# Performance work log

Measured on AMD Instinct MI355X. Metric: run time of the kernel, lower is better.

The kernel has to match this reference:

```python
import jax, jax.numpy as jnp
import numpy as np

EPS = 1e-5
NHEAD = 8
TOP_K = 2


def _layernorm(x, g, b):
    m = jnp.mean(x, axis=-1, keepdims=True)
    v = jnp.mean((x - m) ** 2, axis=-1, keepdims=True)
    return (x - m) * jax.lax.rsqrt(v + EPS) * g + b


def setup_inputs() -> dict:
    S, D, F, E = 4096, 512, 2048, 8
    key = jax.random.key(0)
    ks = jax.random.split(key, 18)
    std = 0.02
    return {
        "src": jax.random.normal(ks[0], (S, D), jnp.float32),
        "in_proj_w": std * jax.random.normal(ks[1], (3 * D, D), jnp.float32),
        "in_proj_b": jnp.zeros((3 * D,), jnp.float32),
        "out_proj_w": std * jax.random.normal(ks[2], (D, D), jnp.float32),
        "out_proj_b": jnp.zeros((D,), jnp.float32),
        "ln1_g": jnp.ones((D,), jnp.float32),
        "ln1_b": jnp.zeros((D,), jnp.float32),
        "ln2_g": jnp.ones((D,), jnp.float32),
        "ln2_b": jnp.zeros((D,), jnp.float32),
        "gate_w": std * jax.random.normal(ks[3], (E, D), jnp.float32),
        "gate_b": jnp.zeros((E,), jnp.float32),
        "w1": std * jax.random.normal(ks[4], (E, F, D), jnp.float32),
        "b1": jnp.zeros((E, F), jnp.float32),
        "w2": std * jax.random.normal(ks[5], (E, F, D), jnp.float32),
        "b2": jnp.zeros((E, F), jnp.float32),
        "wo": std * jax.random.normal(ks[6], (E, D, F), jnp.float32),
        "bo": jnp.zeros((E, D), jnp.float32),
    }


def _sa_block(x, in_proj_w, in_proj_b, out_proj_w, out_proj_b):
    # x: [S, D] unbatched sequence (torch MultiheadAttention unbatched path)
    S, D = x.shape
    hd = D // NHEAD
    qkv = x @ in_proj_w.T + in_proj_b              # [S, 3D]
    q, k, v = jnp.split(qkv, 3, axis=-1)
    q = q.reshape(S, NHEAD, hd)
    k = k.reshape(S, NHEAD, hd)
    v = v.reshape(S, NHEAD, hd)
    scores = jnp.einsum("shd,thd->hst", q, k) / jnp.sqrt(jnp.float32(hd))
    attn = jax.nn.softmax(scores, axis=-1)         # [H, S, S]
    out = jnp.einsum("hst,thd->shd", attn, v).reshape(S, D)
    return out @ out_proj_w.T + out_proj_b


def _ff_block(x, gate_w, gate_b, w1, b1, w2, b2, wo, bo):
    # top-k gated SwiGLU MoE; gate probs are softmax, NOT renormalized after topk
    T = x.shape[0]
    E = w1.shape[0]
    gates = jax.nn.softmax(x @ gate_w.T + gate_b, axis=-1)      # [T, E]
    top_scores, top_idx = jax.lax.top_k(gates, TOP_K)            # [T, k]
    combine = jnp.zeros((T, E), x.dtype).at[
        jnp.arange(T)[:, None], top_idx].add(top_scores)         # [T, E]
    out = jnp.zeros_like(x)
    for e in range(E):  # small fixed expert count
        h = jax.nn.silu(x @ w1[e].T + b1[e]) * (x @ w2[e].T + b2[e])
        out = out + combine[:, e:e + 1] * (h @ wo[e].T + bo[e])
    return out


def reference(src, in_proj_w, in_proj_b, out_proj_w, out_proj_b,
              ln1_g, ln1_b, ln2_g, ln2_b,
              gate_w, gate_b, w1, b1, w2, b2, wo, bo):
    # norm_first pre-norm residual layer, dropout=0 (eval)
    x = src
    x = x + _sa_block(_layernorm(x, ln1_g, ln1_b),
                      in_proj_w, in_proj_b, out_proj_w, out_proj_b)
    x = x + _ff_block(_layernorm(x, ln2_g, ln2_b),
                      gate_w, gate_b, w1, b1, w2, b2, wo, bo)
    return x
```

## Files before the change

### kernel.cpp

```cpp
#include <hip/hip_runtime.h>
#include <hip/hip_bf16.h>
#include <math.h>

#define SQ   4096
#define DM   512
#define NH   8
#define HDIM 64
#define FF   2048
#define NE   8

typedef unsigned short u16;
typedef unsigned int   u32;
typedef __attribute__((ext_vector_type(8))) __bf16 bf16x8;
typedef __attribute__((ext_vector_type(4))) float  f32x4;

__device__ __forceinline__ float bf2f(u16 v) {
    union { u32 i; float f; } c; c.i = ((u32)v) << 16; return c.f;
}
__device__ __forceinline__ u16 f2bf(float f) {
    union { float f; u32 i; } c; c.f = f; u32 u = c.i;
    return (u16)((u + 0x7fffu + ((u >> 16) & 1u)) >> 16);
}

#define BM 128
#define BN 128
#define BK 32
#define BKP 40

__global__ __launch_bounds__(256) void gemm_split(
    const u16* __restrict__ Ahi, const u16* __restrict__ Alo, int lda,
    const u16* __restrict__ Bhi, const u16* __restrict__ Blo, int ldb,
    int M, int N, int K,
    const float* __restrict__ bias,
    const float* __restrict__ resid, int ldres,
    u16* __restrict__ Chi, u16* __restrict__ Clo,
    float* __restrict__ Cf, int ldc, int mode)
{
    __shared__ __align__(16) u16 Ash[BM * BKP], Asl[BM * BKP];
    __shared__ __align__(16) u16 Bsh[BN * BKP], Bsl[BN * BKP];
    const int tid  = threadIdx.x;
    const int wave = tid >> 6;
    const int lane = tid & 63;
    const int quad = lane >> 4;
    const int l16  = lane & 15;
    const int bm = blockIdx.x * BM;
    const int bn = blockIdx.y * BN;
    const int wm = (wave & 1) * 64;
    const int wn = (wave >> 1) * 64;

    f32x4 acc[4][4];
#pragma unroll
    for (int i = 0; i < 4; i++)
#pragma unroll
        for (int j = 0; j < 4; j++)
#pragma unroll
            for (int r = 0; r < 4; r++) acc[i][j][r] = 0.0f;

    for (int k0 = 0; k0 < K; k0 += BK) {
#pragma unroll
        for (int i = 0; i < 2; i++) {
            int c = tid + i * 256;
            int row = c >> 2;
            int col = (c & 3) << 3;
            int ga = bm + row, gb2 = bn + row;
            uint4 vah = make_uint4(0u,0u,0u,0u), val = vah, vbh = vah, vbl = vah;
            if (ga < M) {
                vah = *(const uint4*)(Ahi + (size_t)ga * lda + k0 + col);
                val = *(const uint4*)(Alo + (size_t)ga * lda + k0 + col);
            }
            if (gb2 < N) {
                vbh = *(const uint4*)(Bhi + (size_t)gb2 * ldb + k0 + col);
                vbl = *(const uint4*)(Blo + (size_t)gb2 * ldb + k0 + col);
            }
            *(uint4*)(Ash + row * BKP + col) = vah;
            *(uint4*)(Asl + row * BKP + col) = val;
            *(uint4*)(Bsh + row * BKP + col) = vbh;
            *(uint4*)(Bsl + row * BKP + col) = vbl;
        }
        __syncthreads();
        bf16x8 ah[4], al[4], bh[4], bl[4];
#pragma unroll
        for (int i = 0; i < 4; i++) {
            ah[i] = *(const bf16x8*)(Ash + (wm + i * 16 + l16) * BKP + quad * 8);
            al[i] = *(const bf16x8*)(Asl + (wm + i * 16 + l16) * BKP + quad * 8);
        }
#pragma unroll
        for (int j = 0; j < 4; j++) {
            bh[j] = *(const bf16x8*)(Bsh + (wn + j * 16 + l16) * BKP + quad * 8);
            bl[j] = *(const bf16x8*)(Bsl + (wn + j * 16 + l16) * BKP + quad * 8);
        }
#pragma unroll
        for (int i = 0; i < 4; i++)
#pragma unroll
            for (int j = 0; j < 4; j++) {
                acc[i][j] = __builtin_amdgcn_mfma_f32_16x16x32_bf16(ah[i], bh[j], acc[i][j], 0,0,0);
                acc[i][j] = __builtin_amdgcn_mfma_f32_16x16x32_bf16(ah[i], bl[j], acc[i][j], 0,0,0);
                acc[i][j] = __builtin_amdgcn_mfma_f32_16x16x32_bf16(al[i], bh[j], acc[i][j], 0,0,0);
            }
        __syncthreads();
    }

#pragma unroll
    for (int i = 0; i < 4; i++)
#pragma unroll
        for (int j = 0; j < 4; j++)
#pragma unroll
            for (int r = 0; r < 4; r++) {
                int row = bm + wm + i * 16 + quad * 4 + r;
                int col = bn + wn + j * 16 + l16;
                if (row >= M || col >= N) continue;
                float v = acc[i][j][r] + (bias ? bias[col] : 0.0f);
                size_t idx = (size_t)row * ldc + col;
                if (mode == 0) {
                    u16 hb = f2bf(v);
                    Chi[idx] = hb;
                    Clo[idx] = f2bf(v - bf2f(hb));
                } else {
                    if (resid) v += resid[(size_t)row * ldres + col];
                    Cf[idx] = v;
                }
            }
}

__global__ __launch_bounds__(256) void moe12_all(
    const u16* __restrict__ A, int lda,
    const int* __restrict__ idxl, const int* __restrict__ cnt,
    const int* __restrict__ off,
    const float* __restrict__ w1, const float* __restrict__ b1,
    const float* __restrict__ w2, const float* __restrict__ b2,
    u16* __restrict__ H)
{
    const int bmg = blockIdx.x * BM;
    if (bmg >= off[NE]) return;
    int e = 0;
    while (e < NE - 1 && bmg >= off[e + 1]) e++;
    const int M   = cnt[e];
    const int bml = bmg - off[e];
    if (bml >= M) return;
    const float* B1 = w1 + (size_t)e * FF * DM;
    const float* B2 = w2 + (size_t)e * FF * DM;
    const int*   rl = idxl + e * SQ;

    __shared__ __align__(16) u16 As[BM * BKP], Bs1[BN * BKP], Bs2[BN * BKP];
    const int tid  = threadIdx.x;
    const int wave = tid >> 6;
    const int lane = tid & 63;
    const int quad = lane >> 4;
    const int l16  = lane & 15;
    const int bn = blockIdx.y * BN;
    const int wm = (wave & 1) * 64;
    const int wn = (wave >> 1) * 64;

    f32x4 acc1[4][4], acc2[4][4];
#pragma unroll
    for (int i = 0; i < 4; i++)
#pragma unroll
        for (int j = 0; j < 4; j++)
#pragma unroll
            for (int r = 0; r < 4; r++) { acc1[i][j][r] = 0.0f; acc2[i][j][r] = 0.0f; }

    for (int k0 = 0; k0 < DM; k0 += BK) {
#pragma unroll
        for (int i = 0; i < 2; i++) {
            int c = tid + i * 256;
            int row = c >> 2;
            int col = (c & 3) << 3;
            uint4 va = make_uint4(0u,0u,0u,0u);
            int lr = bml + row;
            if (lr < M) {
                int ar = rl[lr];
                va = *(const uint4*)(A + (size_t)ar * lda + k0 + col);
            }
            *(uint4*)(As + row * BKP + col) = va;
        }
#pragma unroll
        for (int i = 0; i < 4; i++) {
            int c = tid + i * 256;
            int row = c >> 3;
            int col = (c & 7) << 2;
            float4 v1 = *(const float4*)(B1 + (size_t)(bn + row) * DM + k0 + col);
            float4 v2 = *(const float4*)(B2 + (size_t)(bn + row) * DM + k0 + col);
            ushort4 h1, h2;
            h1.x = f2bf(v1.x); h1.y = f2bf(v1.y); h1.z = f2bf(v1.z); h1.w = f2bf(v1.w);
            h2.x = f2bf(v2.x); h2.y = f2bf(v2.y); h2.z = f2bf(v2.z); h2.w = f2bf(v2.w);
            *(ushort4*)(Bs1 + row * BKP + col) = h1;
            *(ushort4*)(Bs2 + row * BKP + col) = h2;
        }
        __syncthreads();
        bf16x8 af[4], b1f[4], b2f[4];
#pragma unroll
        for (int i = 0; i < 4; i++)
            af[i] = *(const bf16x8*)(As + (wm + i * 16 + l16) * BKP + quad * 8);
#pragma unroll
        for (int j = 0; j < 4; j++) {
            b1f[j] = *(const bf16x8*)(Bs1 + (wn + j * 16 + l16) * BKP + quad * 8);
            b2f[j] = *(const bf16x8*)(Bs2 + (wn + j * 16 + l16) * BKP + quad * 8);
        }
#pragma unroll
        for (int i = 0; i < 4; i++)
#pragma unroll
            for (int j = 0; j < 4; j++) {
                acc1[i][j] = __builtin_amdgcn_mfma_f32_16x16x32_bf16(af[i], b1f[j], acc1[i][j], 0,0,0);
                acc2[i][j] = __builtin_amdgcn_mfma_f32_16x16x32_bf16(af[i], b2f[j], acc2[i][j], 0,0,0);
            }
        __syncthreads();
    }

#pragma unroll
    for (int i = 0; i < 4; i++)
#pragma unroll
        for (int j = 0; j < 4; j++)
#pragma unroll
            for (int r = 0; r < 4; r++) {
                int rowl = bml + wm + i * 16 + quad * 4 + r;
                if (rowl >= M) continue;
                int col = bn + wn + j * 16 + l16;
                float g1 = acc1[i][j][r] + b1[e * FF + col];
                float g2 = acc2[i][j][r] + b2[e * FF + col];
                float s  = g1 / (1.0f + __expf(-g1));
                H[(size_t)(off[e] + rowl) * FF + col] = f2bf(s * g2);
            }
}

__global__ __launch_bounds__(256) void moe_y_all(
    const u16* __restrict__ H,
    const float* __restrict__ wo, const float* __restrict__ bo,
    const int* __restrict__ idxl, const float* __restrict__ cw,
    const int* __restrict__ cnt, const int* __restrict__ off,
    float* __restrict__ out)
{
    const int bmg = blockIdx.x * BM;
    if (bmg >= off[NE]) return;
    int e = 0;
    while (e < NE - 1 && bmg >= off[e + 1]) e++;
    const int M   = cnt[e];
    const int bml = bmg - off[e];
    if (bml >= M) return;
    const float* B = wo + (size_t)e * DM * FF;

    __shared__ __align__(16) u16 As[BM * BKP], Bs[BN * BKP];
    const int tid  = threadIdx.x;
    const int wave = tid >> 6;
    const int lane = tid & 63;
    const int quad = lane >> 4;
    const int l16  = lane & 15;
    const int bn = blockIdx.y * BN;
    const int wm = (wave & 1) * 64;
    const int wn = (wave >> 1) * 64;

    f32x4 acc[4][4];
#pragma unroll
    for (int i = 0; i < 4; i++)
#pragma unroll
        for (int j = 0; j < 4; j++)
#pragma unroll
            for (int r = 0; r < 4; r++) acc[i][j][r] = 0.0f;

    for (int k0 = 0; k0 < FF; k0 += BK) {
#pragma unroll
        for (int i = 0; i < 2; i++) {
            int c = tid + i * 256;
            int row = c >> 2;
            int col = (c & 3) << 3;
            uint4 va = *(const uint4*)(H + (size_t)(bmg + row) * FF + k0 + col);
            *(uint4*)(As + row * BKP + col) = va;
        }
#pragma unroll
        for (int i = 0; i < 4; i++) {
            int c = tid + i * 256;
            int row = c >> 3;
            int col = (c & 7) << 2;
            float4 v = *(const float4*)(B + (size_t)(bn + row) * FF + k0 + col);
            ushort4 h;
            h.x = f2bf(v.x); h.y = f2bf(v.y); h.z = f2bf(v.z); h.w = f2bf(v.w);
            *(ushort4*)(Bs + row * BKP + col) = h;
        }
        __syncthreads();
        bf16x8 af[4], bf[4];
#pragma unroll
        for (int i = 0; i < 4; i++)
            af[i] = *(const bf16x8*)(As + (wm + i * 16 + l16) * BKP + quad * 8);
#pragma unroll
        for (int j = 0; j < 4; j++)
            bf[j] = *(const bf16x8*)(Bs + (wn + j * 16 + l16) * BKP + quad * 8);
#pragma unroll
        for (int i = 0; i < 4; i++)
#pragma unroll
            for (int j = 0; j < 4; j++)
                acc[i][j] = __builtin_amdgcn_mfma_f32_16x16x32_bf16(af[i], bf[j], acc[i][j], 0,0,0);
        __syncthreads();
    }

#pragma unroll
    for (int i = 0; i < 4; i++)
#pragma unroll
        for (int j = 0; j < 4; j++)
#pragma unroll
            for (int r = 0; r < 4; r++) {
                int rowl = bml + wm + i * 16 + quad * 4 + r;
                if (rowl >= M) continue;
                int col = bn + wn + j * 16 + l16;
                int tok = idxl[e * SQ + rowl];
                float wgt = cw[e * SQ + rowl];
                atomicAdd(out + (size_t)tok * DM + col,
                          wgt * (acc[i][j][r] + bo[e * DM + col]));
            }
}

#define KP 72
#define SCL 0.18033688011112042f
__global__ __launch_bounds__(256) void flash_attn(
    const u16* __restrict__ qh, const u16* __restrict__ ql,
    const u16* __restrict__ vth, const u16* __restrict__ vtl,
    u16* __restrict__ oh, u16* __restrict__ ol)
{
    __shared__ __align__(16) u16 Ksh[64*KP], Ksl[64*KP], Vsh[64*KP], Vsl[64*KP];
    const int tid  = threadIdx.x;
    const int wave = tid >> 6;
    const int lane = tid & 63;
    const int quad = lane >> 4;
    const int l16  = lane & 15;
    const int h    = blockIdx.y;
    const int qbase = blockIdx.x * 64 + wave * 16;

    u16* const Pwh = Ksh + wave * (16 * KP);
    u16* const Pwl = Ksl + wave * (16 * KP);

    bf16x8 aqh[2], aql[2];
#pragma unroll
    for (int kk = 0; kk < 2; kk++) {
        size_t off = (size_t)(qbase + l16) * (3*DM) + h*HDIM + kk*32 + quad*8;
        aqh[kk] = *(const bf16x8*)(qh + off);
        aql[kk] = *(const bf16x8*)(ql + off);
    }

    float m_[4], l_[4];
    f32x4 o_[4];
#pragma unroll
    for (int r = 0; r < 4; r++) { m_[r] = -1e30f; l_[r] = 0.0f; }
#pragma unroll
    for (int nd = 0; nd < 4; nd++)
#pragma unroll
        for (int r = 0; r < 4; r++) o_[nd][r] = 0.0f;

    for (int jt = 0; jt < SQ / 64; jt++) {
#pragma unroll
        for (int i = 0; i < 2; i++) {
            int c = tid + i * 256;
            int r = c >> 3;
            int co = (c & 7) << 3;
            size_t koff = (size_t)(jt*64 + r) * (3*DM) + DM + h*HDIM + co;
            size_t voff = (size_t)(h*HDIM + r) * SQ + jt*64 + co;
            *(uint4*)(Ksh + r*KP + co) = *(const uint4*)(qh + koff);
            *(uint4*)(Ksl + r*KP + co) = *(const uint4*)(ql + koff);
            *(uint4*)(Vsh + r*KP + co) = *(const uint4*)(vth + voff);
            *(uint4*)(Vsl + r*KP + co) = *(const uint4*)(vtl + voff);
        }
        __syncthreads();

        f32x4 s[4];
#pragma unroll
        for (int jn = 0; jn < 4; jn++) {
            f32x4 z;
#pragma unroll
            for (int r = 0; r < 4; r++) z[r] = 0.0f;
#pragma unroll
            for (int kk = 0; kk < 2; kk++) {
                bf16x8 kh = *(const bf16x8*)(Ksh + (jn*16 + l16)*KP + kk*32 + quad*8);
                bf16x8 kl = *(const bf16x8*)(Ksl + (jn*16 + l16)*KP + kk*32 + quad*8);
                z = __builtin_amdgcn_mfma_f32_16x16x32_bf16(aqh[kk], kh, z, 0,0,0);
                z = __builtin_amdgcn_mfma_f32_16x16x32_bf16(aqh[kk], kl, z, 0,0,0);
                z = __builtin_amdgcn_mfma_f32_16x16x32_bf16(aql[kk], kh, z, 0,0,0);
            }
#pragma unroll
            for (int r = 0; r < 4; r++) z[r] *= SCL;
            s[jn] = z;
        }
        __syncthreads();

        float mx[4], al2[4], rs[4];
#pragma unroll
        for (int r = 0; r < 4; r++)
            mx[r] = fmaxf(fmaxf(s[0][r], s[1][r]), fmaxf(s[2][r], s[3][r]));
#pragma unroll
        for (int r = 0; r < 4; r++) {
#pragma unroll
            for (int o2 = 1; o2 < 16; o2 <<= 1)
                mx[r] = fmaxf(mx[r], __shfl_xor(mx[r], o2));
            float nm = fmaxf(m_[r], mx[r]);
            al2[r] = exp2f(m_[r] - nm);
            m_[r] = nm;
            rs[r] = 0.0f;
        }
#pragma unroll
        for (int jn = 0; jn < 4; jn++)
#pragma unroll
            for (int r = 0; r < 4; r++) {
                float p = exp2f(s[jn][r] - m_[r]);
                s[jn][r] = p;
                rs[r] += p;
            }
#pragma unroll
        for (int r = 0; r < 4; r++) {
#pragma unroll
            for (int o2 = 1; o2 < 16; o2 <<= 1)
                rs[r] += __shfl_xor(rs[r], o2);
            l_[r] = l_[r] * al2[r] + rs[r];
        }
#pragma unroll
        for (int nd = 0; nd < 4; nd++)
#pragma unroll
            for (int r = 0; r < 4; r++) o_[nd][r] *= al2[r];
#pragma unroll
        for (int jn = 0; jn < 4; jn++)
#pragma unroll
            for (int r = 0; r < 4; r++) {
                float p = s[jn][r];
                u16 ph = f2bf(p);
                int pidx = (quad*4 + r)*KP + jn*16 + l16;
                Pwh[pidx] = ph;
                Pwl[pidx] = f2bf(p - bf2f(ph));
            }

        bf16x8 ph[2], pl[2];
#pragma unroll
        for (int kk = 0; kk < 2; kk++) {
            ph[kk] = *(const bf16x8*)(Pwh + l16*KP + kk*32 + quad*8);
            pl[kk] = *(const bf16x8*)(Pwl + l16*KP + kk*32 + quad*8);
        }
#pragma unroll
        for (int nd = 0; nd < 4; nd++) {
#pragma unroll
            for (int kk = 0; kk < 2; kk++) {
                bf16x8 vh = *(const bf16x8*)(Vsh + (nd*16 + l16)*KP + kk*32 + quad*8);
                bf16x8 vl = *(const bf16x8*)(Vsl + (nd*16 + l16)*KP + kk*32 + quad*8);
                o_[nd] = __builtin_amdgcn_mfma_f32_16x16x32_bf16(ph[kk], vh, o_[nd], 0,0,0);
                o_[nd] = __builtin_amdgcn_mfma_f32_16x16x32_bf16(ph[kk], vl, o_[nd], 0,0,0);
                o_[nd] = __builtin_amdgcn_mfma_f32_16x16x32_bf16(pl[kk], vh, o_[nd], 0,0,0);
            }
        }
        __syncthreads();
    }

#pragma unroll
    for (int nd = 0; nd < 4; nd++)
#pragma unroll
        for (int r = 0; r < 4; r++) {
            int row = qbase + quad*4 + r;
            int col = h*HDIM + nd*16 + l16;
            float w = o_[nd][r] / l_[r];
            u16 hb = f2bf(w);
            oh[(size_t)row * DM + col] = hb;
            ol[(size_t)row * DM + col] = f2bf(w - bf2f(hb));
        }
}

__global__ __launch_bounds__(256) void ln1_split(
    const float* __restrict__ x, const float* __restrict__ g,
    const float* __restrict__ b, u16* __restrict__ ohi, u16* __restrict__ olo)
{
    const int row = blockIdx.x;
    const int tid = threadIdx.x;
    float v0 = x[(size_t)row * DM + tid];
    float v1 = x[(size_t)row * DM + tid + 256];
    float s = v0 + v1, sq = v0*v0 + v1*v1;
#pragma unroll
    for (int o = 1; o < 64; o <<= 1) { s += __shfl_xor(s, o); sq += __shfl_xor(sq, o); }
    __shared__ float ss[4], ssq[4];
    if ((tid & 63) == 0) { ss[tid>>6] = s; ssq[tid>>6] = sq; }
    __syncthreads();
    s  = ss[0]+ss[1]+ss[2]+ss[3];
    sq = ssq[0]+ssq[1]+ssq[2]+ssq[3];
    float m = s * (1.0f/DM);
    float rstd = rsqrtf(sq*(1.0f/DM) - m*m + 1e-5f);
    float y0 = (v0-m)*rstd*g[tid]     + b[tid];
    float y1 = (v1-m)*rstd*g[tid+256] + b[tid+256];
    u16 h0 = f2bf(y0), h1 = f2bf(y1);
    ohi[(size_t)row*DM + tid]       = h0;  olo[(size_t)row*DM + tid]       = f2bf(y0 - bf2f(h0));
    ohi[(size_t)row*DM + tid + 256] = h1;  olo[(size_t)row*DM + tid + 256] = f2bf(y1 - bf2f(h1));
}

__global__ __launch_bounds__(256) void ln_kernel(
    const float* __restrict__ x, const float* __restrict__ g,
    const float* __restrict__ b, u16* __restrict__ out)
{
    const int row = blockIdx.x;
    const int tid = threadIdx.x;
    float v0 = x[(size_t)row * DM + tid];
    float v1 = x[(size_t)row * DM + tid + 256];
    float s = v0 + v1, sq = v0*v0 + v1*v1;
#pragma unroll
    for (int o = 1; o < 64; o <<= 1) { s += __shfl_xor(s, o); sq += __shfl_xor(sq, o); }
    __shared__ float ss[4], ssq[4];
    if ((tid & 63) == 0) { ss[tid>>6] = s; ssq[tid>>6] = sq; }
    __syncthreads();
    s  = ss[0]+ss[1]+ss[2]+ss[3];
    sq = ssq[0]+ssq[1]+ssq[2]+ssq[3];
    float m = s * (1.0f/DM);
    float rstd = rsqrtf(sq*(1.0f/DM) - m*m + 1e-5f);
    out[(size_t)row*DM + tid]       = f2bf((v0-m)*rstd*g[tid]     + b[tid]);
    out[(size_t)row*DM + tid + 256] = f2bf((v1-m)*rstd*g[tid+256] + b[tid+256]);
}

__global__ __launch_bounds__(256) void transpose_v2(
    const u16* __restrict__ qh, const u16* __restrict__ ql,
    u16* __restrict__ vth, u16* __restrict__ vtl)
{
    __shared__ u16 Th[64 * 66], Tl[64 * 66];
    const int t0  = blockIdx.x * 64;
    const int hd0 = blockIdx.y * 64;
    const int tid = threadIdx.x;
#pragma unroll
    for (int k = 0; k < 16; k++) {
        int idx = tid + k * 256;
        int r = idx >> 6, j = idx & 63;
        size_t src = (size_t)(t0 + r) * (3*DM) + 2*DM + hd0 + j;
        Th[r * 66 + j] = qh[src];
        Tl[r * 66 + j] = ql[src];
    }
    __syncthreads();
#pragma unroll
    for (int k = 0; k < 16; k++) {
        int idx = tid + k * 256;
        int r = idx >> 6, c2 = idx & 63;
        size_t dst = (size_t)(hd0 + r) * SQ + t0 + c2;
        vth[dst] = Th[c2 * 66 + r];
        vtl[dst] = Tl[c2 * 66 + r];
    }
}

__global__ __launch_bounds__(256) void gate_route(
    const float* __restrict__ x1, const float* __restrict__ g,
    const float* __restrict__ b, const float* __restrict__ gw,
    const float* __restrict__ gb,
    int* __restrict__ cnt, int* __restrict__ idxl, float* __restrict__ cw)
{
    const int token = blockIdx.x * 4 + (threadIdx.x >> 6);
    const int lane  = threadIdx.x & 63;
    const float* xr = x1 + (size_t)token * DM;
    float v[8];
#pragma unroll
    for (int i = 0; i < 8; i++) v[i] = xr[lane*8 + i];
    float s = 0.f, sq = 0.f;
#pragma unroll
    for (int i = 0; i < 8; i++) { s += v[i]; sq += v[i]*v[i]; }
#pragma unroll
    for (int o = 1; o < 64; o <<= 1) { s += __shfl_xor(s, o); sq += __shfl_xor(sq, o); }
    float m = s * (1.0f/DM);
    float rstd = rsqrtf(sq*(1.0f/DM) - m*m + 1e-5f);
    float xn[8];
#pragma unroll
    for (int i = 0; i < 8; i++)
        xn[i] = (v[i]-m)*rstd*g[lane*8+i] + b[lane*8+i];
    float logit[8];
#pragma unroll
    for (int e = 0; e < 8; e++) {
        float t = 0.f;
#pragma unroll
        for (int i = 0; i < 8; i++) t += xn[i] * gw[e*DM + lane*8 + i];
#pragma unroll
        for (int o = 1; o < 64; o <<= 1) t += __shfl_xor(t, o);
        logit[e] = t + gb[e];
    }
    if (lane == 0) {
        float mx = -1e30f;
        for (int e = 0; e < 8; e++) mx = fmaxf(mx, logit[e]);
        float den = 0.f, p[8];
        for (int e = 0; e < 8; e++) { p[e] = __expf(logit[e] - mx); den += p[e]; }
        for (int e = 0; e < 8; e++) p[e] /= den;
        int i1 = 0;
        for (int e = 1; e < 8; e++) if (p[e] > p[i1]) i1 = e;
        int i2 = -1;
        for (int e = 0; e < 8; e++) { if (e == i1) continue; if (i2 < 0 || p[e] > p[i2]) i2 = e; }
        int s1 = atomicAdd(&cnt[i1], 1);
        idxl[i1*SQ + s1] = token;  cw[i1*SQ + s1] = p[i1];
        int s2 = atomicAdd(&cnt[i2], 1);
        idxl[i2*SQ + s2] = token;  cw[i2*SQ + s2] = p[i2];
    }
}

__global__ __launch_bounds__(256) void cvt_split_w(
    const float* __restrict__ w, u16* __restrict__ wh, u16* __restrict__ wl, int n)
{
    int i = blockIdx.x * 256 + threadIdx.x;
    if (i < n) {
        float v = w[i];
        u16 h = f2bf(v);
        wh[i] = h;
        wl[i] = f2bf(v - bf2f(h));
    }
}

__global__ __launch_bounds__(64) void zero_cnt(int* cnt)
{
    if (threadIdx.x < NE) cnt[threadIdx.x] = 0;
}

__global__ __launch_bounds__(64) void make_off(const int* __restrict__ cnt,
                                              int* __restrict__ off)
{
    if (threadIdx.x == 0) {
        int a = 0;
        for (int e = 0; e < NE; e++) {
            off[e] = a;
            a += ((cnt[e] + 127) >> 7) << 7;
        }
        off[NE] = a;
    }
}

__global__ __launch_bounds__(256) void init_out(
    const float* __restrict__ x1, float* __restrict__ out)
{
    int i = blockIdx.x * 256 + threadIdx.x;
    ((float4*)out)[i] = ((const float4*)x1)[i];
}

__global__ __launch_bounds__(256) void sentinel_kernel(float* out, float v, int n)
{
    int i = blockIdx.x * 256 + threadIdx.x;
    if (i < n) out[i] = v;
}
__global__ __launch_bounds__(256) void scrub_kernel(float* out, int n)
{
    int i = blockIdx.x * 256 + threadIdx.x;
    if (i < n) { float v = out[i]; if (!isfinite(v)) out[i] = 777.0f; }
}

extern "C" void kernel_launch(void* const* d_in, const int* in_sizes, int n_in,
                              void* d_out, int out_size, void* d_ws, size_t ws_size,
                              hipStream_t stream)
{
    const float* src        = (const float*)d_in[0];
    const float* in_proj_w  = (const float*)d_in[1];
    const float* in_proj_b  = (const float*)d_in[2];
    const float* out_proj_w = (const float*)d_in[3];
    const float* out_proj_b = (const float*)d_in[4];
    const float* ln1_g      = (const float*)d_in[5];
    const float* ln1_b      = (const float*)d_in[6];
    const float* ln2_g      = (const float*)d_in[7];
    const float* ln2_b      = (const float*)d_in[8];
    const float* gate_w     = (const float*)d_in[9];
    const float* gate_b     = (const float*)d_in[10];
    const float* w1         = (const float*)d_in[11];
    const float* b1         = (const float*)d_in[12];
    const float* w2         = (const float*)d_in[13];
    const float* b2         = (const float*)d_in[14];
    const float* wo         = (const float*)d_in[15];
    const float* bo         = (const float*)d_in[16];
    float* out = (float*)d_out;

    const size_t MB = (size_t)1 << 20;
    const size_t ROUTE = 512 * 1024;
    const size_t NEED = ROUTE + 44 * MB;
    if (ws_size < NEED) {
        sentinel_kernel<<<(SQ*DM)/256, 256, 0, stream>>>(out, 333.0f, SQ*DM);
        return;
    }

    char* ws = (char*)d_ws;
    int*   cnt  = (int*)ws;
    int*   offp = (int*)(ws + 64);
    int*   idxl = (int*)(ws + 1024);
    float* cw   = (float*)(ws + 1024 + 128*1024);
    char*  base = ws + ROUTE;
    u16* xln1h = (u16*)(base);
    u16* xln1l = (u16*)(base + 4*MB);
    u16* attnh = (u16*)(base);
    u16* attnl = (u16*)(base + 4*MB);
    u16* qkvh  = (u16*)(base + 8*MB);
    u16* qkvl  = (u16*)(base + 20*MB);
    float* x1  = (float*)(base + 8*MB);
    u16* vth   = (u16*)(base + 32*MB);
    u16* vtl   = (u16*)(base + 36*MB);
    u16* xln2  = (u16*)(base + 36*MB);
    u16* Hbuf  = (u16*)(base);
    u16* wph   = (u16*)(base + 40*MB);
    u16* wpl   = (u16*)(base + 40*MB + 1536*1024);
    u16* woh   = (u16*)(base + 43*MB);
    u16* wol   = (u16*)(base + 43*MB + 512*1024);

    cvt_split_w<<<(3*DM*DM)/256, 256, 0, stream>>>(in_proj_w,  wph, wpl, 3*DM*DM);
    cvt_split_w<<<(DM*DM)/256,   256, 0, stream>>>(out_proj_w, woh, wol, DM*DM);

    ln1_split<<<SQ, 256, 0, stream>>>(src, ln1_g, ln1_b, xln1h, xln1l);
    gemm_split<<<dim3(32, 12), 256, 0, stream>>>(
        xln1h, xln1l, DM, wph, wpl, DM, SQ, 3*DM, DM,
        in_proj_b, nullptr, 0, qkvh, qkvl, nullptr, 3*DM, 0);
    transpose_v2<<<dim3(SQ/64, DM/64), 256, 0, stream>>>(qkvh, qkvl, vth, vtl);
    flash_attn<<<dim3(SQ/64, NH), 256, 0, stream>>>(qkvh, qkvl, vth, vtl, attnh, attnl);
    gemm_split<<<dim3(32, 4), 256, 0, stream>>>(
        attnh, attnl, DM, woh, wol, DM, SQ, DM, DM,
        out_proj_b, src, DM, nullptr, nullptr, x1, DM, 1);

    ln_kernel<<<SQ, 256, 0, stream>>>(x1, ln2_g, ln2_b, xln2);
    zero_cnt<<<1, 64, 0, stream>>>(cnt);
    gate_route<<<SQ/4, 256, 0, stream>>>(x1, ln2_g, ln2_b, gate_w, gate_b,
                                         cnt, idxl, cw);
    make_off<<<1, 64, 0, stream>>>(cnt, offp);
    init_out<<<(SQ*DM/4)/256, 256, 0, stream>>>(x1, out);
    moe12_all<<<dim3(72, 16), 256, 0, stream>>>(
        xln2, DM, idxl, cnt, offp, w1, b1, w2, b2, Hbuf);
    moe_y_all<<<dim3(72, 4), 256, 0, stream>>>(
        Hbuf, wo, bo, idxl, cw, cnt, offp, out);

    scrub_kernel<<<(SQ*DM)/256, 256, 0, stream>>>(out, SQ*DM);
}
```

Before: 835.7 us.

## Split flash attention over KV sequence into two partitions with combine kernel

Adds a split-KV (flash-decoding style) variant of the attention kernel that launches twice as many blocks, each covering half the key range. Each block writes unnormalized partial outputs plus running max and sum to workspace, and a new combine kernel merges the two partitions and performs the hi/lo bf16 split. This targets low occupancy, since 512 blocks underfill the GPU. The cost is an extra fp32 round-trip of partial outputs and one more launch, and the path only runs when the workspace is at least 61MB beyond the routing area.

```diff
diff --git a/kernel.cpp b/kernel.cpp
--- a/kernel.cpp
+++ b/kernel.cpp
@@ -309,10 +309,14 @@
 
 #define KP 72
 #define SCL 0.18033688011112042f
-__global__ __launch_bounds__(256) void flash_attn(
+
+template <int SPLIT>
+__device__ __forceinline__ void flash_body(
     const u16* __restrict__ qh, const u16* __restrict__ ql,
     const u16* __restrict__ vth, const u16* __restrict__ vtl,
-    u16* __restrict__ oh, u16* __restrict__ ol)
+    u16* __restrict__ oh, u16* __restrict__ ol,
+    float* __restrict__ Opart, float* __restrict__ mpart,
+    float* __restrict__ lpart)
 {
     __shared__ __align__(16) u16 Ksh[64*KP], Ksl[64*KP], Vsh[64*KP], Vsl[64*KP];
     const int tid  = threadIdx.x;
@@ -321,6 +325,7 @@
     const int quad = lane >> 4;
     const int l16  = lane & 15;
     const int h    = blockIdx.y;
+    const int z    = (SPLIT > 1) ? blockIdx.z : 0;
     const int qbase = blockIdx.x * 64 + wave * 16;
 
     u16* const Pwh = Ksh + wave * (16 * KP);
@@ -343,7 +348,8 @@
 #pragma unroll
         for (int r = 0; r < 4; r++) o_[nd][r] = 0.0f;
 
-    for (int jt = 0; jt < SQ / 64; jt++) {
+    const int NT = SQ / 64 / SPLIT;
+    for (int jt = z * NT; jt < (z + 1) * NT; jt++) {
 #pragma unroll
         for (int i = 0; i < 2; i++) {
             int c = tid + i * 256;
@@ -361,20 +367,20 @@
         f32x4 s[4];
 #pragma unroll
         for (int jn = 0; jn < 4; jn++) {
-            f32x4 z;
-#pragma unroll
-            for (int r = 0; r < 4; r++) z[r] = 0.0f;
+            f32x4 zz;
+#pragma unroll
+            for (int r = 0; r < 4; r++) zz[r] = 0.0f;
 #pragma unroll
             for (int kk = 0; kk < 2; kk++) {
                 bf16x8 kh = *(const bf16x8*)(Ksh + (jn*16 + l16)*KP + kk*32 + quad*8);
                 bf16x8 kl = *(const bf16x8*)(Ksl + (jn*16 + l16)*KP + kk*32 + quad*8);
-                z = __builtin_amdgcn_mfma_f32_16x16x32_bf16(aqh[kk], kh, z, 0,0,0);
-                z = __builtin_amdgcn_mfma_f32_16x16x32_bf16(aqh[kk], kl, z, 0,0,0);
-                z = __builtin_amdgcn_mfma_f32_16x16x32_bf16(aql[kk], kh, z, 0,0,0);
-            }
-#pragma unroll
-            for (int r = 0; r < 4; r++) z[r] *= SCL;
-            s[jn] = z;
+                zz = __builtin_amdgcn_mfma_f32_16x16x32_bf16(aqh[kk], kh, zz, 0,0,0);
+                zz = __builtin_amdgcn_mfma_f32_16x16x32_bf16(aqh[kk], kl, zz, 0,0,0);
+                zz = __builtin_amdgcn_mfma_f32_16x16x32_bf16(aql[kk], kh, zz, 0,0,0);
+            }
+#pragma unroll
+            for (int r = 0; r < 4; r++) zz[r] *= SCL;
+            s[jn] = zz;
         }
         __syncthreads();
 
@@ -442,17 +448,81 @@
         __syncthreads();
     }
 
-#pragma unroll
-    for (int nd = 0; nd < 4; nd++)
-#pragma unroll
-        for (int r = 0; r < 4; r++) {
-            int row = qbase + quad*4 + r;
-            int col = h*HDIM + nd*16 + l16;
-            float w = o_[nd][r] / l_[r];
-            u16 hb = f2bf(w);
-            oh[(size_t)row * DM + col] = hb;
-            ol[(size_t)row * DM + col] = f2bf(w - bf2f(hb));
-        }
+    if (SPLIT == 1) {
+#pragma unroll
+        for (int nd = 0; nd < 4; nd++)
+#pragma unroll
+            for (int r = 0; r < 4; r++) {
+                int row = qbase + quad*4 + r;
+                int col = h*HDIM + nd*16 + l16;
+                float w = o_[nd][r] / l_[r];
+                u16 hb = f2bf(w);
+                oh[(size_t)row * DM + col] = hb;
+                ol[(size_t)row * DM + col] = f2bf(w - bf2f(hb));
+            }
+    } else {
+#pragma unroll
+        for (int nd = 0; nd < 4; nd++)
+#pragma unroll
+            for (int r = 0; r < 4; r++) {
+                int row = qbase + quad*4 + r;
+                int col = h*HDIM + nd*16 + l16;
+                Opart[((size_t)z * SQ + row) * DM + col] = o_[nd][r];
+            }
+        if (l16 == 0) {
+#pragma unroll
+            for (int r = 0; r < 4; r++) {
+                int row = qbase + quad*4 + r;
+                mpart[(z*NH + h) * SQ + row] = m_[r];
+                lpart[(z*NH + h) * SQ + row] = l_[r];
+            }
+        }
+    }
+}
+
+__global__ __launch_bounds__(256) void flash_attn(
+    const u16* __restrict__ qh, const u16* __restrict__ ql,
+    const u16* __restrict__ vth, const u16* __restrict__ vtl,
+    u16* __restrict__ oh, u16* __restrict__ ol)
+{
+    flash_body<1>(qh, ql, vth, vtl, oh, ol, nullptr, nullptr, nullptr);
+}
+
+__global__ __launch_bounds__(256) void flash_attn_part(
+    const u16* __restrict__ qh, const u16* __restrict__ ql,
+    const u16* __restrict__ vth, const u16* __restrict__ vtl,
+    float* __restrict__ Opart, float* __restrict__ mpart,
+    float* __restrict__ lpart)
+{
+    flash_body<2>(qh, ql, vth, vtl, nullptr, nullptr, Opart, mpart, lpart);
+}
+
+__global__ __launch_bounds__(256) void attn_combine(
+    const float* __restrict__ Opart, const float* __restrict__ mpart,
+    const float* __restrict__ lpart,
+    u16* __restrict__ oh, u16* __restrict__ ol)
+{
+    const int row = blockIdx.x;
+    const int tid = threadIdx.x;
+#pragma unroll
+    for (int i = 0; i < 2; i++) {
+        int col = tid + i * 256;
+        int h = col >> 6;
+        float m0 = mpart[h * SQ + row];
+        float m1 = mpart[(NH + h) * SQ + row];
+        float l0 = lpart[h * SQ + row];
+        float l1 = lpart[(NH + h) * SQ + row];
+        float m  = fmaxf(m0, m1);
+        float a0 = exp2f(m0 - m);
+        float a1 = exp2f(m1 - m);
+        float O  = Opart[(size_t)row * DM + col] * a0
+                 + Opart[((size_t)SQ + row) * DM + col] * a1;
+        float l  = l0 * a0 + l1 * a1;
+        float w  = O / l;
+        u16 hb = f2bf(w);
+        oh[(size_t)row * DM + col] = hb;
+        ol[(size_t)row * DM + col] = f2bf(w - bf2f(hb));
+    }
 }
 
 __global__ __launch_bounds__(256) void ln1_split(
@@ -652,11 +722,13 @@
 
     const size_t MB = (size_t)1 << 20;
     const size_t ROUTE = 512 * 1024;
-    const size_t NEED = ROUTE + 44 * MB;
+    const size_t NEED     = ROUTE + 44 * MB;
+    const size_t NEED_BIG = ROUTE + 61 * MB;
     if (ws_size < NEED) {
         sentinel_kernel<<<(SQ*DM)/256, 256, 0, stream>>>(out, 333.0f, SQ*DM);
         return;
     }
+    const bool big = (ws_size >= NEED_BIG);
 
     char* ws = (char*)d_ws;
     int*   cnt  = (int*)ws;
@@ -679,6 +751,9 @@
     u16* wpl   = (u16*)(base + 40*MB + 1536*1024);
     u16* woh   = (u16*)(base + 43*MB);
     u16* wol   = (u16*)(base + 43*MB + 512*1024);
+    float* Opart = (float*)(base + 44*MB);
+    float* mpart = (float*)(base + 60*MB);
+    float* lpart = (float*)(base + 60*MB + 256*1024);
 
     cvt_split_w<<<(3*DM*DM)/256, 256, 0, stream>>>(in_proj_w,  wph, wpl, 3*DM*DM);
     cvt_split_w<<<(DM*DM)/256,   256, 0, stream>>>(out_proj_w, woh, wol, DM*DM);
@@ -688,7 +763,14 @@
         xln1h, xln1l, DM, wph, wpl, DM, SQ, 3*DM, DM,
         in_proj_b, nullptr, 0, qkvh, qkvl, nullptr, 3*DM, 0);
     transpose_v2<<<dim3(SQ/64, DM/64), 256, 0, stream>>>(qkvh, qkvl, vth, vtl);
-    flash_attn<<<dim3(SQ/64, NH), 256, 0, stream>>>(qkvh, qkvl, vth, vtl, attnh, attnl);
+    if (big) {
+        flash_attn_part<<<dim3(SQ/64, NH, 2), 256, 0, stream>>>(
+            qkvh, qkvl, vth, vtl, Opart, mpart, lpart);
+        attn_combine<<<SQ, 256, 0, stream>>>(Opart, mpart, lpart, attnh, attnl);
+    } else {
+        flash_attn<<<dim3(SQ/64, NH), 256, 0, stream>>>(
+            qkvh, qkvl, vth, vtl, attnh, attnl);
+    }
     gemm_split<<<dim3(32, 4), 256, 0, stream>>>(
         attnh, attnl, DM, woh, wol, DM, SQ, DM, DM,
         out_proj_b, src, DM, nullptr, nullptr, x1, DM, 1);
```

Result: no change. 819.8 us (-1.9%).
